# Kernel optimization log

Hardware: AMD Instinct MI355X
Metric: run time of the kernel (lower is better)

Reference implementation:

```python
import jax, jax.numpy as jnp
import numpy as np

N_NODES = 100000
N_EDGES = 200000
N_ATOM_FEATS = 56
HIDDEN = 256
N_GRAPHS = 2048
OUT_DIM = 1
EPS = 1e-5  # torch BatchNorm1d default


def setup_inputs() -> dict:
    key = jax.random.key(0)
    ks = jax.random.split(key, 10)
    x = jax.random.randint(ks[0], (N_NODES, N_ATOM_FEATS), 0, 2, dtype=jnp.int64 if jax.config.jax_enable_x64 else jnp.int32)
    edge_index = jax.random.randint(ks[1], (2, N_EDGES), 0, N_NODES)
    batch = jnp.sort(jax.random.randint(ks[2], (N_NODES,), 0, N_GRAPHS))
    emb_tables = jax.random.normal(ks[3], (N_ATOM_FEATS, 2, HIDDEN), dtype=jnp.float32) * 0.1
    Ws = jax.random.normal(ks[4], (3, HIDDEN, HIDDEN), dtype=jnp.float32) * (1.0 / np.sqrt(HIDDEN))
    bs = jnp.zeros((3, HIDDEN), dtype=jnp.float32)
    gammas = jnp.ones((2, HIDDEN), dtype=jnp.float32)
    betas = jnp.zeros((2, HIDDEN), dtype=jnp.float32)
    lin_w = jax.random.normal(ks[5], (HIDDEN, OUT_DIM), dtype=jnp.float32) * (1.0 / np.sqrt(HIDDEN))
    lin_b = jnp.zeros((OUT_DIM,), dtype=jnp.float32)
    return {"x": x, "edge_index": edge_index, "batch": batch, "emb_tables": emb_tables,
            "Ws": Ws, "bs": bs, "gammas": gammas, "betas": betas, "lin_w": lin_w, "lin_b": lin_b}


def reference(x, edge_index, batch, emb_tables, Ws, bs, gammas, betas, lin_w, lin_b):
    n = x.shape[0]
    # --- AtomEncoder: sum of 56 per-feature embedding lookups ---
    # emb_tables: [56, 2, H]; x: [N, 56] -> gathered [N, 56, H] -> sum over feature axis
    feat_idx = jnp.arange(x.shape[1])[None, :]  # [1,56]
    h = emb_tables[feat_idx, x].sum(axis=1)      # [N, H]

    # --- GCN normalization with self-loops (shared across layers) ---
    loops = jnp.arange(n)
    src = jnp.concatenate([edge_index[0], loops])
    dst = jnp.concatenate([edge_index[1], loops])
    deg = jax.ops.segment_sum(jnp.ones_like(src, dtype=h.dtype), dst, num_segments=n)
    dinv = jnp.where(deg > 0, jax.lax.rsqrt(deg), 0.0)
    norm = dinv[src] * dinv[dst]  # [E+N]

    def gcn_conv(h, W, b):
        hw = h @ W                                   # [N, H']
        msg = hw[src] * norm[:, None]                # gather + scale
        agg = jax.ops.segment_sum(msg, dst, num_segments=n)  # scatter-add
        return agg + b

    # --- layers 0..L-2: conv -> batchnorm (batch stats) -> relu; eval => no dropout ---
    for i in range(2):
        h = gcn_conv(h, Ws[i], bs[i])
        mu = h.mean(axis=0)
        var = h.var(axis=0)
        h = (h - mu) * jax.lax.rsqrt(var + EPS) * gammas[i] + betas[i]
        h = jax.nn.relu(h)
    # --- last conv (return_embeds=True: no softmax) ---
    h = gcn_conv(h, Ws[2], bs[2])

    # --- global mean pool over graphs ---
    sums = jax.ops.segment_sum(h, batch, num_segments=N_GRAPHS)          # [G, H]
    counts = jax.ops.segment_sum(jnp.ones((n,), h.dtype), batch, num_segments=N_GRAPHS)
    pooled = sums / jnp.maximum(counts, 1.0)[:, None]

    return pooled @ lin_w + lin_b  # [G, OUT_DIM]
```

## Files before the change

kernel.cpp:

```cpp
#include <hip/hip_runtime.h>
#include <hip/hip_bf16.h>

#define NN 100000
#define NE 200000
#define NF 56
#define HD 256
#define NG 2048

#define SCAN_CH 512
#define NCH ((NN + SCAN_CH - 1) / SCAN_CH)
#define EB ((NE + 255) / 256)

#define AB 2048
#define ZB 98
#define CVB ((NN + 255) / 256)
#define ENB ((NN + 127) / 128)

typedef __bf16 bf16x8 __attribute__((ext_vector_type(8)));
typedef __bf16 bf16x4 __attribute__((ext_vector_type(4)));
typedef float  floatx4 __attribute__((ext_vector_type(4)));

__global__ void prep_params(const float* __restrict__ emb, const float* __restrict__ Ws,
                            const float* __restrict__ bs, const float* __restrict__ lw,
                            __bf16* __restrict__ dW0t,
                            float* __restrict__ w2lw, float* __restrict__ b2lw,
                            __bf16* __restrict__ Wt, unsigned* __restrict__ deg,
                            const int* __restrict__ x, __bf16* __restrict__ xb) {
    __shared__ float row[HD];
    int c = threadIdx.x;
    int f = blockIdx.x;
    if (f >= NF + 2) {
        int g = f - (NF + 2);
        if (g < HD) {
            Wt[(size_t)g * HD + c] = (__bf16)Ws[(size_t)HD * HD + (size_t)c * HD + g];
        } else if (g < HD + ZB) {
            int idx = (g - HD) * HD + c;
            if (idx < NN / 4) ((int4*)deg)[idx] = make_int4(0, 0, 0, 0);
        } else {
            int r = (g - HD - ZB) * 256 + c;
            if (r < NN) {
                const int* xr = x + (size_t)r * NF;
                __bf16 o[64];
                #pragma unroll
                for (int j = 0; j < 14; ++j) {
                    int4 iv = *(const int4*)&xr[j * 4];
                    o[j * 4 + 0] = (__bf16)(float)iv.x;
                    o[j * 4 + 1] = (__bf16)(float)iv.y;
                    o[j * 4 + 2] = (__bf16)(float)iv.z;
                    o[j * 4 + 3] = (__bf16)(float)iv.w;
                }
                o[56] = (__bf16)1.0f;
                #pragma unroll
                for (int j = 57; j < 64; ++j) o[j] = (__bf16)0.0f;
                #pragma unroll
                for (int j = 0; j < 8; ++j)
                    *(bf16x8*)&xb[(size_t)r * 64 + j * 8] = *(const bf16x8*)&o[j * 8];
            }
        }
        return;
    }
    if (f == NF + 1) {
        const float* W2 = Ws + (size_t)2 * HD * HD;
        float acc = 0.f;
        for (int k = 0; k < HD; ++k) acc += W2[(size_t)c * HD + k] * lw[k];
        w2lw[c] = acc;
        row[c] = bs[2 * HD + c] * lw[c];
        __syncthreads();
        for (int off = 128; off > 0; off >>= 1) {
            if (c < off) row[c] += row[c + off];
            __syncthreads();
        }
        if (c == 0) *b2lw = row[0];
        return;
    }
    if (f < NF) {
        row[c] = emb[(f * 2 + 1) * HD + c] - emb[(f * 2 + 0) * HD + c];
    } else {
        float s = 0.f;
        for (int ff = 0; ff < NF; ++ff) s += emb[(ff * 2) * HD + c];
        row[c] = s;
    }
    __syncthreads();
    float acc = 0.f;
    for (int k = 0; k < HD; ++k) acc += row[k] * Ws[k * HD + c];
    if (f < NF) {
        dW0t[c * 64 + f] = (__bf16)acc;
    } else {
        dW0t[c * 64 + 56] = (__bf16)acc;
        #pragma unroll
        for (int k = 57; k < 64; ++k) dW0t[c * 64 + k] = (__bf16)0.f;
    }
}

__global__ void deg_kernel(const int* __restrict__ dst, unsigned* __restrict__ deg, int E) {
    int e = blockIdx.x * blockDim.x + threadIdx.x;
    if (e < E) atomicAdd(&deg[dst[e]], 1u);
}

__global__ void chunk_sum_dinv(const unsigned* __restrict__ deg, unsigned* __restrict__ csum,
                               float* __restrict__ dinv, float* __restrict__ selfn) {
    __shared__ unsigned s[SCAN_CH];
    int t = threadIdx.x;
    int base = blockIdx.x * SCAN_CH;
    unsigned v = (base + t < NN) ? deg[base + t] : 0u;
    s[t] = v;
    if (base + t < NN) {
        float d = (float)(v + 1u);
        dinv[base + t]  = rsqrtf(d);
        selfn[base + t] = 1.0f / d;
    }
    __syncthreads();
    for (int off = SCAN_CH / 2; off > 0; off >>= 1) {
        if (t < off) s[t] += s[t + off];
        __syncthreads();
    }
    if (t == 0) csum[blockIdx.x] = s[0];
}

__global__ void chunk_apply(const unsigned* __restrict__ deg, const unsigned* __restrict__ csum,
                            unsigned* __restrict__ row_start, unsigned* __restrict__ cursor) {
    __shared__ unsigned s[SCAN_CH];
    __shared__ unsigned cs[256];
    int t = threadIdx.x;
    if (t < 256) cs[t] = (t < NCH) ? csum[t] : 0u;
    __syncthreads();
    for (int off = 1; off < 256; off <<= 1) {
        unsigned add = (t < 256 && t >= off) ? cs[t - off] : 0u;
        __syncthreads();
        if (t < 256) cs[t] += add;
        __syncthreads();
    }
    unsigned chunk_base = (blockIdx.x == 0) ? 0u : cs[blockIdx.x - 1];

    int base = blockIdx.x * SCAN_CH;
    unsigned v = (base + t < NN) ? deg[base + t] : 0u;
    s[t] = v;
    __syncthreads();
    for (int off = 1; off < SCAN_CH; off <<= 1) {
        unsigned add = (t >= off) ? s[t - off] : 0u;
        __syncthreads();
        s[t] += add;
        __syncthreads();
    }
    if (base + t < NN) {
        unsigned rs = chunk_base + s[t] - v;
        row_start[base + t] = rs;
        cursor[base + t] = rs;
    }
    if (blockIdx.x == 0 && t == 0) row_start[NN] = NE;
}

__global__ void csr_fill_gb(const int* __restrict__ src, const int* __restrict__ dst,
                            const float* __restrict__ dinv, unsigned* __restrict__ cursor,
                            int* __restrict__ ecol, float* __restrict__ enorm,
                            const int* __restrict__ batch, unsigned* __restrict__ gstart) {
    int t = threadIdx.x;
    if (blockIdx.x < EB) {
        int e = blockIdx.x * 256 + t;
        if (e < NE) {
            int s = src[e], d = dst[e];
            unsigned pos = atomicAdd(&cursor[d], 1u);
            ecol[pos] = s;
            enorm[pos] = dinv[s] * dinv[d];
        }
    } else {
        int g = (blockIdx.x - EB) * 256 + t;
        if (g <= NG) {
            int lo = 0, hi = NN;
            while (lo < hi) {
                int mid = (lo + hi) >> 1;
                if (batch[mid] < g) lo = mid + 1; else hi = mid;
            }
            gstart[g] = (unsigned)lo;
        }
    }
}

__global__ void __launch_bounds__(256) agg_x(const __bf16* __restrict__ xb,
                                             const float* __restrict__ selfn,
                                             const unsigned* __restrict__ row_start,
                                             const int* __restrict__ ecol,
                                             const float* __restrict__ enorm,
                                             __bf16* __restrict__ ax) {
    int tid = blockIdx.x * 256 + threadIdx.x;
    int n = tid >> 6;
    if (n >= NN) return;
    int l = tid & 63;
    float acc = (float)xb[(size_t)n * 64 + l] * selfn[n];
    unsigned e0 = row_start[n], e1 = row_start[n + 1];
    unsigned e = e0;
    for (; e + 2 <= e1; e += 2) {
        int s0 = ecol[e], s1 = ecol[e + 1];
        float n0 = enorm[e], n1 = enorm[e + 1];
        float v0 = (float)xb[(size_t)s0 * 64 + l];
        float v1 = (float)xb[(size_t)s1 * 64 + l];
        acc += v0 * n0 + v1 * n1;
    }
    if (e < e1)
        acc += (float)xb[(size_t)ecol[e] * 64 + l] * enorm[e];
    ax[(size_t)n * 64 + l] = (__bf16)acc;
}

#define ELSTR 68
__global__ void __launch_bounds__(512) enc_gemm(const __bf16* __restrict__ ax,
                                                const __bf16* __restrict__ dW0t,
                                                const float* __restrict__ b0,
                                                __bf16* __restrict__ C,
                                                float* __restrict__ part) {
    __shared__ __bf16 sA[128 * ELSTR];
    __shared__ __bf16 sB[256 * ELSTR];
    __shared__ float psum[8][64];
    __shared__ float psq[8][64];
    int t = threadIdx.x;
    int m0 = blockIdx.x * 128;
    int lane = t & 63, w = t >> 6;
    int quad = lane >> 4, l16 = lane & 15;
    int mw = (w & 1) * 64, nw = (w >> 1) * 64;

    {
        int r = t >> 2;
        int k = (t & 3) * 16;
        int row = m0 + r;
        bf16x8 v0 = {}, v1 = {};
        if (row < NN) {
            v0 = *(const bf16x8*)&ax[(size_t)row * 64 + k];
            v1 = *(const bf16x8*)&ax[(size_t)row * 64 + k + 8];
        }
        *(bf16x8*)&sA[r * ELSTR + k]     = v0;
        *(bf16x8*)&sA[r * ELSTR + k + 8] = v1;
    }
    {
        int bn = t >> 1;
        int kh = (t & 1) * 32;
        #pragma unroll
        for (int j = 0; j < 4; ++j)
            *(bf16x8*)&sB[bn * ELSTR + kh + j * 8] =
                *(const bf16x8*)&dW0t[(size_t)bn * 64 + kh + j * 8];
    }
    __syncthreads();

    floatx4 acc[4][4] = {};
    #pragma unroll
    for (int s = 0; s < 2; ++s) {
        bf16x8 af[4], bfr[4];
        #pragma unroll
        for (int i = 0; i < 4; ++i)
            af[i] = *(const bf16x8*)&sA[(mw + i * 16 + l16) * ELSTR + s * 32 + quad * 8];
        #pragma unroll
        for (int i = 0; i < 4; ++i)
            bfr[i] = *(const bf16x8*)&sB[(nw + i * 16 + l16) * ELSTR + s * 32 + quad * 8];
        #pragma unroll
        for (int mi = 0; mi < 4; ++mi)
            #pragma unroll
            for (int ni = 0; ni < 4; ++ni)
                acc[mi][ni] = __builtin_amdgcn_mfma_f32_16x16x32_bf16(
                    af[mi], bfr[ni], acc[mi][ni], 0, 0, 0);
    }

    float bw[4];
    #pragma unroll
    for (int ni = 0; ni < 4; ++ni) bw[ni] = b0[nw + ni * 16 + l16];
    float ls[4] = {0.f, 0.f, 0.f, 0.f};
    float lq[4] = {0.f, 0.f, 0.f, 0.f};
    #pragma unroll
    for (int mi = 0; mi < 4; ++mi) {
        #pragma unroll
        for (int r = 0; r < 4; ++r) {
            int row = m0 + mw + mi * 16 + quad * 4 + r;
            if (row < NN) {
                #pragma unroll
                for (int ni = 0; ni < 4; ++ni) {
                    float v = acc[mi][ni][r] + bw[ni];
                    C[(size_t)row * HD + nw + ni * 16 + l16] = (__bf16)v;
                    ls[ni] += v;
                    lq[ni] += v * v;
                }
            }
        }
    }
    #pragma unroll
    for (int ni = 0; ni < 4; ++ni) {
        ls[ni] += __shfl_xor(ls[ni], 16, 64);
        ls[ni] += __shfl_xor(ls[ni], 32, 64);
        lq[ni] += __shfl_xor(lq[ni], 16, 64);
        lq[ni] += __shfl_xor(lq[ni], 32, 64);
    }
    if (lane < 16) {
        #pragma unroll
        for (int ni = 0; ni < 4; ++ni) {
            psum[w][ni * 16 + l16] = ls[ni];
            psq[w][ni * 16 + l16]  = lq[ni];
        }
    }
    __syncthreads();
    if (!(w & 1) && lane < 16) {
        #pragma unroll
        for (int ni = 0; ni < 4; ++ni) {
            int ci = ni * 16 + l16;
            part[(size_t)blockIdx.x * 512 + nw + ci]       = psum[w][ci] + psum[w + 1][ci];
            part[(size_t)blockIdx.x * 512 + 256 + nw + ci] = psq[w][ci]  + psq[w + 1][ci];
        }
    }
}

#define LSTR 36
__global__ void __launch_bounds__(512) gemm_mfma(const __bf16* __restrict__ A,
                                                 const __bf16* __restrict__ Wt,
                                                 __bf16* __restrict__ C, int M,
                                                 const float* __restrict__ ascale,
                                                 const float* __restrict__ ashift) {
    __shared__ __bf16 sA[128 * LSTR];
    __shared__ __bf16 sB[256 * LSTR];
    int t = threadIdx.x;
    int m0 = blockIdx.x * 128;
    int lane = t & 63, w = t >> 6;
    int quad = lane >> 4, l16 = lane & 15;
    int mw = (w & 1) * 64;
    int nw = (w >> 1) * 64;

    int ar = t >> 2;
    int ak = (t & 3) * 8;
    int bn = t >> 1;
    int bk = (t & 1) * 16;

    auto ldA = [&](int k0, bf16x8& pa) {
        float4 s0 = *(const float4*)&ascale[k0 + ak];
        float4 s1 = *(const float4*)&ascale[k0 + ak + 4];
        float4 h0 = *(const float4*)&ashift[k0 + ak];
        float4 h1 = *(const float4*)&ashift[k0 + ak + 4];
        int row = m0 + ar;
        bf16x8 a = {};
        if (row < M) a = *(const bf16x8*)&A[(size_t)row * HD + k0 + ak];
        bf16x8 b;
        b[0] = (__bf16)fmaxf((float)a[0] * s0.x + h0.x, 0.f);
        b[1] = (__bf16)fmaxf((float)a[1] * s0.y + h0.y, 0.f);
        b[2] = (__bf16)fmaxf((float)a[2] * s0.z + h0.z, 0.f);
        b[3] = (__bf16)fmaxf((float)a[3] * s0.w + h0.w, 0.f);
        b[4] = (__bf16)fmaxf((float)a[4] * s1.x + h1.x, 0.f);
        b[5] = (__bf16)fmaxf((float)a[5] * s1.y + h1.y, 0.f);
        b[6] = (__bf16)fmaxf((float)a[6] * s1.z + h1.z, 0.f);
        b[7] = (__bf16)fmaxf((float)a[7] * s1.w + h1.w, 0.f);
        pa = b;
    };
    auto ldB = [&](int k0, bf16x8 pb[2]) {
        #pragma unroll
        for (int j = 0; j < 2; ++j)
            pb[j] = *(const bf16x8*)&Wt[(size_t)bn * HD + k0 + bk + j * 8];
    };

    bf16x8 pa, pb[2];
    ldA(0, pa);
    ldB(0, pb);

    floatx4 acc[4][4] = {};

    for (int k0 = 0; k0 < 256; k0 += 32) {
        *(bf16x8*)&sA[ar * LSTR + ak] = pa;
        *(bf16x8*)&sB[bn * LSTR + bk]     = pb[0];
        *(bf16x8*)&sB[bn * LSTR + bk + 8] = pb[1];
        __syncthreads();

        if (k0 + 32 < 256) {
            ldA(k0 + 32, pa);
            ldB(k0 + 32, pb);
        }

        bf16x8 af[4], bfr[4];
        #pragma unroll
        for (int i = 0; i < 4; ++i)
            af[i] = *(const bf16x8*)&sA[(mw + i * 16 + l16) * LSTR + quad * 8];
        #pragma unroll
        for (int i = 0; i < 4; ++i)
            bfr[i] = *(const bf16x8*)&sB[(nw + i * 16 + l16) * LSTR + quad * 8];
        #pragma unroll
        for (int mi = 0; mi < 4; ++mi)
            #pragma unroll
            for (int ni = 0; ni < 4; ++ni)
                acc[mi][ni] = __builtin_amdgcn_mfma_f32_16x16x32_bf16(
                    af[mi], bfr[ni], acc[mi][ni], 0, 0, 0);
        __syncthreads();
    }

    #pragma unroll
    for (int mi = 0; mi < 4; ++mi) {
        #pragma unroll
        for (int r = 0; r < 4; ++r) {
            int row = m0 + mw + mi * 16 + quad * 4 + r;
            if (row < M) {
                #pragma unroll
                for (int ni = 0; ni < 4; ++ni)
                    C[(size_t)row * HD + nw + ni * 16 + l16] = (__bf16)acc[mi][ni][r];
            }
        }
    }
}

__global__ void __launch_bounds__(256) gcn_aggregate(const __bf16* __restrict__ hw,
                                                     const float* __restrict__ selfn,
                                                     const float* __restrict__ bias,
                                                     const unsigned* __restrict__ row_start,
                                                     const int* __restrict__ ecol,
                                                     const float* __restrict__ enorm,
                                                     __bf16* __restrict__ agg,
                                                     float* __restrict__ part) {
    int t = threadIdx.x;
    int l = t & 63, w = t >> 6;
    int c4 = l * 4;
    float4 bv = *(const float4*)&bias[c4];
    float4 lsum = make_float4(0.f, 0.f, 0.f, 0.f);
    float4 lssq = make_float4(0.f, 0.f, 0.f, 0.f);

    for (int n = blockIdx.x * 4 + w; n < NN; n += AB * 4) {
        float s = selfn[n];
        bf16x4 hv = *(const bf16x4*)&hw[(size_t)n * HD + c4];
        float4 acc;
        acc.x = (float)hv[0] * s + bv.x;
        acc.y = (float)hv[1] * s + bv.y;
        acc.z = (float)hv[2] * s + bv.z;
        acc.w = (float)hv[3] * s + bv.w;
        unsigned e0 = row_start[n], e1 = row_start[n + 1];
        unsigned e = e0;
        for (; e + 4 <= e1; e += 4) {
            int sv0 = ecol[e], sv1 = ecol[e + 1], sv2 = ecol[e + 2], sv3 = ecol[e + 3];
            float nm0 = enorm[e], nm1 = enorm[e + 1], nm2 = enorm[e + 2], nm3 = enorm[e + 3];
            bf16x4 u0 = *(const bf16x4*)&hw[(size_t)sv0 * HD + c4];
            bf16x4 u1 = *(const bf16x4*)&hw[(size_t)sv1 * HD + c4];
            bf16x4 u2 = *(const bf16x4*)&hw[(size_t)sv2 * HD + c4];
            bf16x4 u3 = *(const bf16x4*)&hw[(size_t)sv3 * HD + c4];
            acc.x += (float)u0[0] * nm0 + (float)u1[0] * nm1 + (float)u2[0] * nm2 + (float)u3[0] * nm3;
            acc.y += (float)u0[1] * nm0 + (float)u1[1] * nm1 + (float)u2[1] * nm2 + (float)u3[1] * nm3;
            acc.z += (float)u0[2] * nm0 + (float)u1[2] * nm1 + (float)u2[2] * nm2 + (float)u3[2] * nm3;
            acc.w += (float)u0[3] * nm0 + (float)u1[3] * nm1 + (float)u2[3] * nm2 + (float)u3[3] * nm3;
        }
        for (; e + 2 <= e1; e += 2) {
            int sv0 = ecol[e], sv1 = ecol[e + 1];
            float nm0 = enorm[e], nm1 = enorm[e + 1];
            bf16x4 u0 = *(const bf16x4*)&hw[(size_t)sv0 * HD + c4];
            bf16x4 u1 = *(const bf16x4*)&hw[(size_t)sv1 * HD + c4];
            acc.x += (float)u0[0] * nm0 + (float)u1[0] * nm1;
            acc.y += (float)u0[1] * nm0 + (float)u1[1] * nm1;
            acc.z += (float)u0[2] * nm0 + (float)u1[2] * nm1;
            acc.w += (float)u0[3] * nm0 + (float)u1[3] * nm1;
        }
        if (e < e1) {
            int sv = ecol[e];
            float nm = enorm[e];
            bf16x4 u = *(const bf16x4*)&hw[(size_t)sv * HD + c4];
            acc.x += (float)u[0] * nm;
            acc.y += (float)u[1] * nm;
            acc.z += (float)u[2] * nm;
            acc.w += (float)u[3] * nm;
        }
        bf16x4 o;
        o[0] = (__bf16)acc.x; o[1] = (__bf16)acc.y;
        o[2] = (__bf16)acc.z; o[3] = (__bf16)acc.w;
        *(bf16x4*)&agg[(size_t)n * HD + c4] = o;

        lsum.x += acc.x; lsum.y += acc.y; lsum.z += acc.z; lsum.w += acc.w;
        lssq.x += acc.x * acc.x; lssq.y += acc.y * acc.y;
        lssq.z += acc.z * acc.z; lssq.w += acc.w * acc.w;
    }

    __shared__ float4 ssum[4][64];
    __shared__ float4 sss[4][64];
    ssum[w][l] = lsum;
    sss[w][l]  = lssq;
    __syncthreads();
    if (w == 0) {
        float4 a0 = ssum[0][l], a1 = ssum[1][l], a2 = ssum[2][l], a3 = ssum[3][l];
        float4 q0 = sss[0][l],  q1 = sss[1][l],  q2 = sss[2][l],  q3 = sss[3][l];
        float4 sm, sq;
        sm.x = a0.x + a1.x + a2.x + a3.x;
        sm.y = a0.y + a1.y + a2.y + a3.y;
        sm.z = a0.z + a1.z + a2.z + a3.z;
        sm.w = a0.w + a1.w + a2.w + a3.w;
        sq.x = q0.x + q1.x + q2.x + q3.x;
        sq.y = q0.y + q1.y + q2.y + q3.y;
        sq.z = q0.z + q1.z + q2.z + q3.z;
        sq.w = q0.w + q1.w + q2.w + q3.w;
        *(float4*)&part[(size_t)blockIdx.x * 512 + c4]       = sm;
        *(float4*)&part[(size_t)blockIdx.x * 512 + 256 + c4] = sq;
    }
}

__global__ void __launch_bounds__(256) bn_scale(const float* __restrict__ part, int nb,
                                                const float* __restrict__ gamma,
                                                const float* __restrict__ beta,
                                                float* __restrict__ scale,
                                                float* __restrict__ shift) {
    __shared__ float rs[256], rq[256];
    int t = threadIdx.x;
    int c = blockIdx.x;
    float s = 0.f, q = 0.f;
    for (int j = t; j < nb; j += 256) {
        s += part[(size_t)j * 512 + c];
        q += part[(size_t)j * 512 + 256 + c];
    }
    rs[t] = s; rq[t] = q;
    __syncthreads();
    for (int off = 128; off > 0; off >>= 1) {
        if (t < off) { rs[t] += rs[t + off]; rq[t] += rq[t + off]; }
        __syncthreads();
    }
    if (t == 0) {
        const float inv_n = 1.0f / (float)NN;
        float mu  = rs[0] * inv_n;
        float var = rq[0] * inv_n - mu * mu;
        float rstd = rsqrtf(var + 1e-5f);
        float sc = gamma[c] * rstd;
        scale[c] = sc;
        shift[c] = beta[c] - mu * sc;
    }
}

__global__ void __launch_bounds__(256) bn_dot(const __bf16* __restrict__ h,
                                              const float* __restrict__ scale,
                                              const float* __restrict__ shift,
                                              const float* __restrict__ w2lw,
                                              float* __restrict__ z) {
    int tid = blockIdx.x * 256 + threadIdx.x;
    int n = tid >> 6;
    if (n >= NN) return;
    int l = tid & 63;
    int c4 = l * 4;
    bf16x4 a = *(const bf16x4*)&h[(size_t)n * HD + c4];
    float4 sc = *(const float4*)&scale[c4];
    float4 sh = *(const float4*)&shift[c4];
    float4 wv = *(const float4*)&w2lw[c4];
    float d = fmaxf((float)a[0] * sc.x + sh.x, 0.f) * wv.x
            + fmaxf((float)a[1] * sc.y + sh.y, 0.f) * wv.y
            + fmaxf((float)a[2] * sc.z + sh.z, 0.f) * wv.z
            + fmaxf((float)a[3] * sc.w + sh.w, 0.f) * wv.w;
    #pragma unroll
    for (int off = 32; off > 0; off >>= 1) d += __shfl_down(d, off, 64);
    if (l == 0) z[n] = d;
}

__global__ void __launch_bounds__(256) pool_fused(const float* __restrict__ z,
                                                  const float* __restrict__ selfn,
                                                  const float* __restrict__ b2lw,
                                                  const unsigned* __restrict__ row_start,
                                                  const int* __restrict__ ecol,
                                                  const float* __restrict__ enorm,
                                                  const unsigned* __restrict__ gstart,
                                                  const float* __restrict__ lb,
                                                  float* __restrict__ out) {
    int tid = blockIdx.x * 256 + threadIdx.x;
    int g = tid >> 6;
    if (g >= NG) return;
    int l = tid & 63;
    unsigned s0 = gstart[g], s1 = gstart[g + 1];
    float bb = *b2lw;
    float s = 0.f;
    for (unsigned i = s0 + l; i < s1; i += 64) {
        float d = selfn[i] * z[i] + bb;
        unsigned e0 = row_start[i], e1 = row_start[i + 1];
        for (unsigned e = e0; e < e1; ++e)
            d += enorm[e] * z[ecol[e]];
        s += d;
    }
    #pragma unroll
    for (int off = 32; off > 0; off >>= 1) s += __shfl_down(s, off, 64);
    if (l == 0) out[g] = s / fmaxf((float)(s1 - s0), 1.0f) + lb[0];
}

extern "C" void kernel_launch(void* const* d_in, const int* in_sizes, int n_in,
                              void* d_out, int out_size, void* d_ws, size_t ws_size,
                              hipStream_t stream) {
    const int*   x     = (const int*)d_in[0];
    const int*   ei    = (const int*)d_in[1];
    const int*   batch = (const int*)d_in[2];
    const float* emb   = (const float*)d_in[3];
    const float* Ws    = (const float*)d_in[4];
    const float* bs    = (const float*)d_in[5];
    const float* gam   = (const float*)d_in[6];
    const float* bet   = (const float*)d_in[7];
    const float* lw    = (const float*)d_in[8];
    const float* lb    = (const float*)d_in[9];
    float* out = (float*)d_out;

    const int* src = ei;
    const int* dst = ei + NE;

    char* p = (char*)d_ws;
    size_t off = 0;
    auto carve = [&](size_t bytes) { void* r = p + off; off = (off + bytes + 255) & ~(size_t)255; return r; };
    __bf16*   buf0   = (__bf16*)carve((size_t)NN * HD * 2);
    __bf16*   buf1   = (__bf16*)carve((size_t)NN * HD * 2);
    __bf16*   xb     = (__bf16*)carve((size_t)NN * 64 * 2);
    __bf16*   ax     = (__bf16*)carve((size_t)NN * 64 * 2);
    __bf16*   dW0t   = (__bf16*)carve(HD * 64 * 2);
    __bf16*   Wt     = (__bf16*)carve((size_t)HD * HD * 2);
    float*    w2lw   = (float*)carve(HD * 4);
    float*    b2lw   = (float*)carve(256);
    unsigned* deg    = (unsigned*)carve(NN * 4);
    float*    dinv   = (float*)carve(NN * 4);
    float*    selfn  = (float*)carve(NN * 4);
    unsigned* csum   = (unsigned*)carve(256 * 4);
    unsigned* row_s  = (unsigned*)carve((NN + 1) * 4);
    unsigned* cursor = (unsigned*)carve(NN * 4);
    int*      ecol   = (int*)carve(NE * 4);
    float*    enorm  = (float*)carve(NE * 4);
    float*    part   = (float*)carve((size_t)AB * 512 * 4);
    float*    scale  = (float*)carve(HD * 4);
    float*    shift  = (float*)carve(HD * 4);
    unsigned* gstart = (unsigned*)carve((NG + 1) * 4);
    float*    zbuf   = (float*)carve(NN * 4);
    (void)ws_size; (void)n_in; (void)in_sizes; (void)out_size;

    prep_params<<<NF + 2 + HD + ZB + CVB, HD, 0, stream>>>(
        emb, Ws, bs, lw, dW0t, w2lw, b2lw, Wt, deg, x, xb);

    deg_kernel<<<(NE + 255) / 256, 256, 0, stream>>>(dst, deg, NE);
    chunk_sum_dinv<<<NCH, SCAN_CH, 0, stream>>>(deg, csum, dinv, selfn);
    chunk_apply<<<NCH, SCAN_CH, 0, stream>>>(deg, csum, row_s, cursor);
    csr_fill_gb<<<EB + (NG + 256) / 256, 256, 0, stream>>>(
        src, dst, dinv, cursor, ecol, enorm, batch, gstart);

    agg_x<<<(NN * 64 + 255) / 256, 256, 0, stream>>>(
        xb, selfn, row_s, ecol, enorm, ax);
    enc_gemm<<<ENB, 512, 0, stream>>>(ax, dW0t, bs, buf0, part);
    bn_scale<<<HD, 256, 0, stream>>>(part, ENB, gam, bet, scale, shift);

    gemm_mfma<<<ENB, 512, 0, stream>>>(buf0, Wt, buf1, NN, scale, shift);
    gcn_aggregate<<<AB, 256, 0, stream>>>(
        buf1, selfn, bs + HD, row_s, ecol, enorm, buf0, part);
    bn_scale<<<HD, 256, 0, stream>>>(part, AB, gam + HD, bet + HD, scale, shift);

    bn_dot<<<(NN * 64 + 255) / 256, 256, 0, stream>>>(buf0, scale, shift, w2lw, zbuf);
    pool_fused<<<(NG * 64 + 255) / 256, 256, 0, stream>>>(
        zbuf, selfn, b2lw, row_s, ecol, enorm, gstart, lb, out);
}
```

Measured before the change: 274.1 us.

## Fuse CSR build, encoder aggregation, and final pooling into cooperative kernels

Merges the degree count, scan, CSR fill and graph-boundary search into one cooperative kernel with grid syncs, replacing four launches and the deg memset. Folds the neighbour aggregation of the one-hot features into the encoder GEMM's shared-memory load, which removes the intermediate ax buffer. Merges bn_dot and pool_fused into one cooperative kernel. The aim is to cut launch overhead and intermediate traffic, at the cost of grid-wide barriers and cooperative launch constraints.

```diff
diff --git a/kernel.cpp b/kernel.cpp
--- a/kernel.cpp
+++ b/kernel.cpp
@@ -1,5 +1,8 @@
 #include <hip/hip_runtime.h>
 #include <hip/hip_bf16.h>
+#include <hip/hip_cooperative_groups.h>
+
+namespace cg = cooperative_groups;
 
 #define NN 100000
 #define NE 200000
@@ -9,12 +12,11 @@
 
 #define SCAN_CH 512
 #define NCH ((NN + SCAN_CH - 1) / SCAN_CH)
-#define EB ((NE + 255) / 256)
 
 #define AB 2048
-#define ZB 98
 #define CVB ((NN + 255) / 256)
 #define ENB ((NN + 127) / 128)
+#define FB 1024
 
 typedef __bf16 bf16x8 __attribute__((ext_vector_type(8)));
 typedef __bf16 bf16x4 __attribute__((ext_vector_type(4)));
@@ -24,7 +26,7 @@
                             const float* __restrict__ bs, const float* __restrict__ lw,
                             __bf16* __restrict__ dW0t,
                             float* __restrict__ w2lw, float* __restrict__ b2lw,
-                            __bf16* __restrict__ Wt, unsigned* __restrict__ deg,
+                            __bf16* __restrict__ Wt,
                             const int* __restrict__ x, __bf16* __restrict__ xb) {
     __shared__ float row[HD];
     int c = threadIdx.x;
@@ -33,11 +35,8 @@
         int g = f - (NF + 2);
         if (g < HD) {
             Wt[(size_t)g * HD + c] = (__bf16)Ws[(size_t)HD * HD + (size_t)c * HD + g];
-        } else if (g < HD + ZB) {
-            int idx = (g - HD) * HD + c;
-            if (idx < NN / 4) ((int4*)deg)[idx] = make_int4(0, 0, 0, 0);
         } else {
-            int r = (g - HD - ZB) * 256 + c;
+            int r = (g - HD) * 256 + c;
             if (r < NN) {
                 const int* xr = x + (size_t)r * NF;
                 __bf16 o[64];
@@ -92,36 +91,53 @@
     }
 }
 
-__global__ void deg_kernel(const int* __restrict__ dst, unsigned* __restrict__ deg, int E) {
-    int e = blockIdx.x * blockDim.x + threadIdx.x;
-    if (e < E) atomicAdd(&deg[dst[e]], 1u);
-}
-
-__global__ void chunk_sum_dinv(const unsigned* __restrict__ deg, unsigned* __restrict__ csum,
-                               float* __restrict__ dinv, float* __restrict__ selfn) {
-    __shared__ unsigned s[SCAN_CH];
-    int t = threadIdx.x;
-    int base = blockIdx.x * SCAN_CH;
-    unsigned v = (base + t < NN) ? deg[base + t] : 0u;
-    s[t] = v;
-    if (base + t < NN) {
-        float d = (float)(v + 1u);
-        dinv[base + t]  = rsqrtf(d);
-        selfn[base + t] = 1.0f / d;
-    }
-    __syncthreads();
-    for (int off = SCAN_CH / 2; off > 0; off >>= 1) {
-        if (t < off) s[t] += s[t + off];
-        __syncthreads();
-    }
-    if (t == 0) csum[blockIdx.x] = s[0];
-}
-
-__global__ void chunk_apply(const unsigned* __restrict__ deg, const unsigned* __restrict__ csum,
-                            unsigned* __restrict__ row_start, unsigned* __restrict__ cursor) {
+__global__ void __launch_bounds__(512) build_csr(const int* __restrict__ src,
+                                                 const int* __restrict__ dst,
+                                                 unsigned* __restrict__ deg,
+                                                 float* __restrict__ dinv,
+                                                 float* __restrict__ selfn,
+                                                 unsigned* __restrict__ csum,
+                                                 unsigned* __restrict__ row_start,
+                                                 unsigned* __restrict__ cursor,
+                                                 int* __restrict__ ecol,
+                                                 float* __restrict__ enorm,
+                                                 const int* __restrict__ batch,
+                                                 unsigned* __restrict__ gstart) {
+    cg::grid_group gg = cg::this_grid();
     __shared__ unsigned s[SCAN_CH];
     __shared__ unsigned cs[256];
     int t = threadIdx.x;
+    int b = blockIdx.x;
+    int gid = b * SCAN_CH + t;
+
+    if (gid < NN) deg[gid] = 0u;
+    gg.sync();
+
+    {
+        int e = gid;
+        #pragma unroll
+        for (int it = 0; it < 2; ++it) {
+            if (e < NE) atomicAdd(&deg[dst[e]], 1u);
+            e += NCH * SCAN_CH;
+        }
+    }
+    gg.sync();
+
+    unsigned v = (gid < NN) ? deg[gid] : 0u;
+    if (gid < NN) {
+        float d = (float)(v + 1u);
+        dinv[gid]  = rsqrtf(d);
+        selfn[gid] = 1.0f / d;
+    }
+    s[t] = v;
+    __syncthreads();
+    for (int off = SCAN_CH / 2; off > 0; off >>= 1) {
+        if (t < off) s[t] += s[t + off];
+        __syncthreads();
+    }
+    if (t == 0) csum[b] = s[0];
+    gg.sync();
+
     if (t < 256) cs[t] = (t < NCH) ? csum[t] : 0u;
     __syncthreads();
     for (int off = 1; off < 256; off <<= 1) {
@@ -130,10 +146,7 @@
         if (t < 256) cs[t] += add;
         __syncthreads();
     }
-    unsigned chunk_base = (blockIdx.x == 0) ? 0u : cs[blockIdx.x - 1];
-
-    int base = blockIdx.x * SCAN_CH;
-    unsigned v = (base + t < NN) ? deg[base + t] : 0u;
+    unsigned chunk_base = (b == 0) ? 0u : cs[b - 1];
     s[t] = v;
     __syncthreads();
     for (int off = 1; off < SCAN_CH; off <<= 1) {
@@ -142,71 +155,47 @@
         s[t] += add;
         __syncthreads();
     }
-    if (base + t < NN) {
+    if (gid < NN) {
         unsigned rs = chunk_base + s[t] - v;
-        row_start[base + t] = rs;
-        cursor[base + t] = rs;
-    }
-    if (blockIdx.x == 0 && t == 0) row_start[NN] = NE;
-}
-
-__global__ void csr_fill_gb(const int* __restrict__ src, const int* __restrict__ dst,
-                            const float* __restrict__ dinv, unsigned* __restrict__ cursor,
-                            int* __restrict__ ecol, float* __restrict__ enorm,
-                            const int* __restrict__ batch, unsigned* __restrict__ gstart) {
-    int t = threadIdx.x;
-    if (blockIdx.x < EB) {
-        int e = blockIdx.x * 256 + t;
-        if (e < NE) {
-            int s = src[e], d = dst[e];
-            unsigned pos = atomicAdd(&cursor[d], 1u);
-            ecol[pos] = s;
-            enorm[pos] = dinv[s] * dinv[d];
-        }
-    } else {
-        int g = (blockIdx.x - EB) * 256 + t;
-        if (g <= NG) {
-            int lo = 0, hi = NN;
-            while (lo < hi) {
-                int mid = (lo + hi) >> 1;
-                if (batch[mid] < g) lo = mid + 1; else hi = mid;
-            }
-            gstart[g] = (unsigned)lo;
-        }
-    }
-}
-
-__global__ void __launch_bounds__(256) agg_x(const __bf16* __restrict__ xb,
-                                             const float* __restrict__ selfn,
-                                             const unsigned* __restrict__ row_start,
-                                             const int* __restrict__ ecol,
-                                             const float* __restrict__ enorm,
-                                             __bf16* __restrict__ ax) {
-    int tid = blockIdx.x * 256 + threadIdx.x;
-    int n = tid >> 6;
-    if (n >= NN) return;
-    int l = tid & 63;
-    float acc = (float)xb[(size_t)n * 64 + l] * selfn[n];
-    unsigned e0 = row_start[n], e1 = row_start[n + 1];
-    unsigned e = e0;
-    for (; e + 2 <= e1; e += 2) {
-        int s0 = ecol[e], s1 = ecol[e + 1];
-        float n0 = enorm[e], n1 = enorm[e + 1];
-        float v0 = (float)xb[(size_t)s0 * 64 + l];
-        float v1 = (float)xb[(size_t)s1 * 64 + l];
-        acc += v0 * n0 + v1 * n1;
-    }
-    if (e < e1)
-        acc += (float)xb[(size_t)ecol[e] * 64 + l] * enorm[e];
-    ax[(size_t)n * 64 + l] = (__bf16)acc;
+        row_start[gid] = rs;
+        cursor[gid] = rs;
+    }
+    if (gid == 0) row_start[NN] = NE;
+    gg.sync();
+
+    {
+        int e = gid;
+        #pragma unroll
+        for (int it = 0; it < 2; ++it) {
+            if (e < NE) {
+                int sv = src[e], dv = dst[e];
+                unsigned pos = atomicAdd(&cursor[dv], 1u);
+                ecol[pos] = sv;
+                enorm[pos] = dinv[sv] * dinv[dv];
+            }
+            e += NCH * SCAN_CH;
+        }
+    }
+    if (gid <= NG) {
+        int lo = 0, hi = NN;
+        while (lo < hi) {
+            int mid = (lo + hi) >> 1;
+            if (batch[mid] < gid) lo = mid + 1; else hi = mid;
+        }
+        gstart[gid] = (unsigned)lo;
+    }
 }
 
 #define ELSTR 68
-__global__ void __launch_bounds__(512) enc_gemm(const __bf16* __restrict__ ax,
-                                                const __bf16* __restrict__ dW0t,
-                                                const float* __restrict__ b0,
-                                                __bf16* __restrict__ C,
-                                                float* __restrict__ part) {
+__global__ void __launch_bounds__(512) enc_fused(const __bf16* __restrict__ xb,
+                                                 const __bf16* __restrict__ dW0t,
+                                                 const float* __restrict__ b0,
+                                                 const float* __restrict__ selfn,
+                                                 const unsigned* __restrict__ row_start,
+                                                 const int* __restrict__ ecol,
+                                                 const float* __restrict__ enorm,
+                                                 __bf16* __restrict__ C,
+                                                 float* __restrict__ part) {
     __shared__ __bf16 sA[128 * ELSTR];
     __shared__ __bf16 sB[256 * ELSTR];
     __shared__ float psum[8][64];
@@ -218,24 +207,61 @@
     int mw = (w & 1) * 64, nw = (w >> 1) * 64;
 
     {
-        int r = t >> 2;
-        int k = (t & 3) * 16;
-        int row = m0 + r;
-        bf16x8 v0 = {}, v1 = {};
-        if (row < NN) {
-            v0 = *(const bf16x8*)&ax[(size_t)row * 64 + k];
-            v1 = *(const bf16x8*)&ax[(size_t)row * 64 + k + 8];
-        }
-        *(bf16x8*)&sA[r * ELSTR + k]     = v0;
-        *(bf16x8*)&sA[r * ELSTR + k + 8] = v1;
-    }
-    {
         int bn = t >> 1;
         int kh = (t & 1) * 32;
         #pragma unroll
         for (int j = 0; j < 4; ++j)
             *(bf16x8*)&sB[bn * ELSTR + kh + j * 8] =
                 *(const bf16x8*)&dW0t[(size_t)bn * 64 + kh + j * 8];
+    }
+    {
+        int r = t >> 2;
+        int p = (t & 3) * 16;
+        int n = m0 + r;
+        float acc[16];
+        #pragma unroll
+        for (int i = 0; i < 16; ++i) acc[i] = 0.f;
+        if (n < NN) {
+            float sn = selfn[n];
+            bf16x8 a0 = *(const bf16x8*)&xb[(size_t)n * 64 + p];
+            bf16x8 a1 = *(const bf16x8*)&xb[(size_t)n * 64 + p + 8];
+            #pragma unroll
+            for (int i = 0; i < 8; ++i) {
+                acc[i]     = (float)a0[i] * sn;
+                acc[8 + i] = (float)a1[i] * sn;
+            }
+            unsigned e0 = row_start[n], e1 = row_start[n + 1];
+            unsigned e = e0;
+            for (; e + 2 <= e1; e += 2) {
+                int s0 = ecol[e], s1 = ecol[e + 1];
+                float n0v = enorm[e], n1v = enorm[e + 1];
+                bf16x8 u00 = *(const bf16x8*)&xb[(size_t)s0 * 64 + p];
+                bf16x8 u01 = *(const bf16x8*)&xb[(size_t)s0 * 64 + p + 8];
+                bf16x8 u10 = *(const bf16x8*)&xb[(size_t)s1 * 64 + p];
+                bf16x8 u11 = *(const bf16x8*)&xb[(size_t)s1 * 64 + p + 8];
+                #pragma unroll
+                for (int i = 0; i < 8; ++i) {
+                    acc[i]     += (float)u00[i] * n0v + (float)u10[i] * n1v;
+                    acc[8 + i] += (float)u01[i] * n0v + (float)u11[i] * n1v;
+                }
+            }
+            if (e < e1) {
+                int s0 = ecol[e];
+                float n0v = enorm[e];
+                bf16x8 u00 = *(const bf16x8*)&xb[(size_t)s0 * 64 + p];
+                bf16x8 u01 = *(const bf16x8*)&xb[(size_t)s0 * 64 + p + 8];
+                #pragma unroll
+                for (int i = 0; i < 8; ++i) {
+                    acc[i]     += (float)u00[i] * n0v;
+                    acc[8 + i] += (float)u01[i] * n0v;
+                }
+            }
+        }
+        bf16x8 o0, o1;
+        #pragma unroll
+        for (int i = 0; i < 8; ++i) { o0[i] = (__bf16)acc[i]; o1[i] = (__bf16)acc[8 + i]; }
+        *(bf16x8*)&sA[r * ELSTR + p]     = o0;
+        *(bf16x8*)&sA[r * ELSTR + p + 8] = o1;
     }
     __syncthreads();
 
@@ -513,55 +539,57 @@
     }
 }
 
-__global__ void __launch_bounds__(256) bn_dot(const __bf16* __restrict__ h,
-                                              const float* __restrict__ scale,
-                                              const float* __restrict__ shift,
-                                              const float* __restrict__ w2lw,
-                                              float* __restrict__ z) {
-    int tid = blockIdx.x * 256 + threadIdx.x;
-    int n = tid >> 6;
-    if (n >= NN) return;
-    int l = tid & 63;
+__global__ void __launch_bounds__(256, 4) final_fused(const __bf16* __restrict__ h,
+                                                      const float* __restrict__ scale,
+                                                      const float* __restrict__ shift,
+                                                      const float* __restrict__ w2lw,
+                                                      float* __restrict__ z,
+                                                      const float* __restrict__ selfn,
+                                                      const float* __restrict__ b2lw,
+                                                      const unsigned* __restrict__ row_start,
+                                                      const int* __restrict__ ecol,
+                                                      const float* __restrict__ enorm,
+                                                      const unsigned* __restrict__ gstart,
+                                                      const float* __restrict__ lb,
+                                                      float* __restrict__ out) {
+    cg::grid_group gg = cg::this_grid();
+    int t = threadIdx.x;
+    int l = t & 63, w = t >> 6;
     int c4 = l * 4;
-    bf16x4 a = *(const bf16x4*)&h[(size_t)n * HD + c4];
-    float4 sc = *(const float4*)&scale[c4];
-    float4 sh = *(const float4*)&shift[c4];
-    float4 wv = *(const float4*)&w2lw[c4];
-    float d = fmaxf((float)a[0] * sc.x + sh.x, 0.f) * wv.x
-            + fmaxf((float)a[1] * sc.y + sh.y, 0.f) * wv.y
-            + fmaxf((float)a[2] * sc.z + sh.z, 0.f) * wv.z
-            + fmaxf((float)a[3] * sc.w + sh.w, 0.f) * wv.w;
-    #pragma unroll
-    for (int off = 32; off > 0; off >>= 1) d += __shfl_down(d, off, 64);
-    if (l == 0) z[n] = d;
-}
-
-__global__ void __launch_bounds__(256) pool_fused(const float* __restrict__ z,
-                                                  const float* __restrict__ selfn,
-                                                  const float* __restrict__ b2lw,
-                                                  const unsigned* __restrict__ row_start,
-                                                  const int* __restrict__ ecol,
-                                                  const float* __restrict__ enorm,
-                                                  const unsigned* __restrict__ gstart,
-                                                  const float* __restrict__ lb,
-                                                  float* __restrict__ out) {
-    int tid = blockIdx.x * 256 + threadIdx.x;
-    int g = tid >> 6;
-    if (g >= NG) return;
-    int l = tid & 63;
-    unsigned s0 = gstart[g], s1 = gstart[g + 1];
-    float bb = *b2lw;
-    float s = 0.f;
-    for (unsigned i = s0 + l; i < s1; i += 64) {
-        float d = selfn[i] * z[i] + bb;
-        unsigned e0 = row_start[i], e1 = row_start[i + 1];
-        for (unsigned e = e0; e < e1; ++e)
-            d += enorm[e] * z[ecol[e]];
-        s += d;
-    }
-    #pragma unroll
-    for (int off = 32; off > 0; off >>= 1) s += __shfl_down(s, off, 64);
-    if (l == 0) out[g] = s / fmaxf((float)(s1 - s0), 1.0f) + lb[0];
+    {
+        float4 sc = *(const float4*)&scale[c4];
+        float4 sh = *(const float4*)&shift[c4];
+        float4 wv = *(const float4*)&w2lw[c4];
+        for (int n = blockIdx.x * 4 + w; n < NN; n += FB * 4) {
+            bf16x4 a = *(const bf16x4*)&h[(size_t)n * HD + c4];
+            float d = fmaxf((float)a[0] * sc.x + sh.x, 0.f) * wv.x
+                    + fmaxf((float)a[1] * sc.y + sh.y, 0.f) * wv.y
+                    + fmaxf((float)a[2] * sc.z + sh.z, 0.f) * wv.z
+                    + fmaxf((float)a[3] * sc.w + sh.w, 0.f) * wv.w;
+            #pragma unroll
+            for (int off = 32; off > 0; off >>= 1) d += __shfl_down(d, off, 64);
+            if (l == 0) z[n] = d;
+        }
+    }
+    gg.sync();
+    {
+        int g = blockIdx.x * 2 + w;
+        if (w < 2 && g < NG) {
+            unsigned s0 = gstart[g], s1 = gstart[g + 1];
+            float bb = *b2lw;
+            float s = 0.f;
+            for (unsigned i = s0 + l; i < s1; i += 64) {
+                float d = selfn[i] * z[i] + bb;
+                unsigned e0 = row_start[i], e1 = row_start[i + 1];
+                for (unsigned e = e0; e < e1; ++e)
+                    d += enorm[e] * z[ecol[e]];
+                s += d;
+            }
+            #pragma unroll
+            for (int off = 32; off > 0; off >>= 1) s += __shfl_down(s, off, 64);
+            if (l == 0) out[g] = s / fmaxf((float)(s1 - s0), 1.0f) + lb[0];
+        }
+    }
 }
 
 extern "C" void kernel_launch(void* const* d_in, const int* in_sizes, int n_in,
@@ -588,7 +616,6 @@
     __bf16*   buf0   = (__bf16*)carve((size_t)NN * HD * 2);
     __bf16*   buf1   = (__bf16*)carve((size_t)NN * HD * 2);
     __bf16*   xb     = (__bf16*)carve((size_t)NN * 64 * 2);
-    __bf16*   ax     = (__bf16*)carve((size_t)NN * 64 * 2);
     __bf16*   dW0t   = (__bf16*)carve(HD * 64 * 2);
     __bf16*   Wt     = (__bf16*)carve((size_t)HD * HD * 2);
     float*    w2lw   = (float*)carve(HD * 4);
@@ -608,18 +635,19 @@
     float*    zbuf   = (float*)carve(NN * 4);
     (void)ws_size; (void)n_in; (void)in_sizes; (void)out_size;
 
-    prep_params<<<NF + 2 + HD + ZB + CVB, HD, 0, stream>>>(
-        emb, Ws, bs, lw, dW0t, w2lw, b2lw, Wt, deg, x, xb);
-
-    deg_kernel<<<(NE + 255) / 256, 256, 0, stream>>>(dst, deg, NE);
-    chunk_sum_dinv<<<NCH, SCAN_CH, 0, stream>>>(deg, csum, dinv, selfn);
-    chunk_apply<<<NCH, SCAN_CH, 0, stream>>>(deg, csum, row_s, cursor);
-    csr_fill_gb<<<EB + (NG + 256) / 256, 256, 0, stream>>>(
-        src, dst, dinv, cursor, ecol, enorm, batch, gstart);
-
-    agg_x<<<(NN * 64 + 255) / 256, 256, 0, stream>>>(
-        xb, selfn, row_s, ecol, enorm, ax);
-    enc_gemm<<<ENB, 512, 0, stream>>>(ax, dW0t, bs, buf0, part);
+    prep_params<<<NF + 2 + HD + CVB, HD, 0, stream>>>(
+        emb, Ws, bs, lw, dW0t, w2lw, b2lw, Wt, x, xb);
+
+    {
+        void* args[] = {(void*)&src, (void*)&dst, (void*)&deg, (void*)&dinv, (void*)&selfn,
+                        (void*)&csum, (void*)&row_s, (void*)&cursor, (void*)&ecol,
+                        (void*)&enorm, (void*)&batch, (void*)&gstart};
+        hipLaunchCooperativeKernel(reinterpret_cast<void*>(build_csr),
+                                   dim3(NCH), dim3(SCAN_CH), args, 0, stream);
+    }
+
+    enc_fused<<<ENB, 512, 0, stream>>>(
+        xb, dW0t, bs, selfn, row_s, ecol, enorm, buf0, part);
     bn_scale<<<HD, 256, 0, stream>>>(part, ENB, gam, bet, scale, shift);
 
     gemm_mfma<<<ENB, 512, 0, stream>>>(buf0, Wt, buf1, NN, scale, shift);
@@ -627,7 +655,11 @@
         buf1, selfn, bs + HD, row_s, ecol, enorm, buf0, part);
     bn_scale<<<HD, 256, 0, stream>>>(part, AB, gam + HD, bet + HD, scale, shift);
 
-    bn_dot<<<(NN * 64 + 255) / 256, 256, 0, stream>>>(buf0, scale, shift, w2lw, zbuf);
-    pool_fused<<<(NG * 64 + 255) / 256, 256, 0, stream>>>(
-        zbuf, selfn, b2lw, row_s, ecol, enorm, gstart, lb, out);
-}
+    {
+        void* args[] = {(void*)&buf0, (void*)&scale, (void*)&shift, (void*)&w2lw,
+                        (void*)&zbuf, (void*)&selfn, (void*)&b2lw, (void*)&row_s,
+                        (void*)&ecol, (void*)&enorm, (void*)&gstart, (void*)&lb, (void*)&out};
+        hipLaunchCooperativeKernel(reinterpret_cast<void*>(final_fused),
+                                   dim3(FB), dim3(256), args, 0, stream);
+    }
+}
```

Result: slower. 412.7 us (+50.6%).
